# Kernel tuning notes

Measured on AMD Instinct MI355X. Metric: run time of the kernel, lower is better.

## Reference

```python
import jax, jax.numpy as jnp
import numpy as np

N_USERS = 10000
N_ITEMS = 100000
N_FEATURES = 64
EMB_DIM = 128
TAU = 0.01
NUM_SEQ = 100000
SEQ_LEN = 50


def setup_inputs() -> dict:
    key = jax.random.key(0)
    k1, k2, k3, k4, k5, k6 = jax.random.split(key, 6)
    users = jax.random.randint(k1, (NUM_SEQ,), 0, N_USERS, dtype=jnp.int32)
    items = jax.random.randint(k2, (NUM_SEQ,), 0, N_ITEMS, dtype=jnp.int32)
    R_ui = jax.random.normal(k3, (NUM_SEQ, SEQ_LEN, N_FEATURES), dtype=jnp.float32)
    mask = jax.random.randint(k4, (NUM_SEQ, SEQ_LEN), 0, 2).astype(bool)
    mask = mask.at[:, 0].set(True)  # ensure every sequence has >=1 valid step
    w = jax.random.normal(k5, (N_FEATURES,), dtype=jnp.float32)  # nn.init.normal_
    item_emb = jax.random.normal(k6, (N_ITEMS + 1, EMB_DIM), dtype=jnp.float32) * 0.1
    item_emb = item_emb.at[0].set(0.0)  # padding_idx=0
    alpha = jnp.ones((1,), jnp.float32)
    beta = jnp.ones((1,), jnp.float32)
    gamma = jnp.ones((1,), jnp.float32)
    return {"users": users, "items": items, "R_ui": R_ui, "mask": mask,
            "w": w, "item_emb": item_emb, "alpha": alpha, "beta": beta, "gamma": gamma}


def reference(users, items, R_ui, mask, w, item_emb, alpha, beta, gamma):
    # Z: [num_seq, seq_len] masked power-mean features
    Z = jnp.einsum('nsd,d->ns', R_ui, w)
    Wv = jnp.maximum(Z, TAU)                       # nn.Threshold(tau, tau)
    Wp = jnp.where(mask, Wv ** alpha, 0.0)         # W[~mask] = 0, then **alpha
    W_alpha = jnp.sum(Wp, axis=-1) ** (1.0 / alpha)
    R_beta = jnp.sum(mask, axis=-1).astype(R_ui.dtype) ** beta
    wt = (W_alpha * R_beta) ** gamma               # [num_seq]
    q = item_emb[items]                            # [num_seq, emb_dim]
    # per-user weighted average (replaces Python loop over users.unique())
    num = jax.ops.segment_sum(wt[:, None] * q, users, num_segments=N_USERS + 1)
    den = jax.ops.segment_sum(wt, users, num_segments=N_USERS + 1)
    p = num[users] / den[users][:, None]
    r = jnp.sum(p * q, axis=-1)                    # [num_seq]
    return r
```

## Files before the change

### kernel.cpp

```cpp
#include <hip/hip_runtime.h>
#include <hip/hip_bf16.h>
#include <stdint.h>

#define N_USERS   10000
#define N_ITEMS   100000
#define N_FEAT    64
#define EMB_DIM   128
#define SEQ_LEN   50
#define TAU       0.01f

typedef float f32x4 __attribute__((ext_vector_type(4)));

__device__ inline f32x4 nt_load4(const float* p) {
    return __builtin_nontemporal_load(reinterpret_cast<const f32x4*>(p));
}


__device__ inline int detect_mask_mode(const void* mask_raw, int lane) {
    const unsigned int* mi = (const unsigned int*)mask_raw;
    unsigned int pv = mi[lane];
    float        pf = __uint_as_float(pv);
    bool allint = __all(pv <= 1u) != 0;
    bool allflt = __all(pf == 0.0f || pf == 1.0f) != 0;
    return allint ? 0 : (allflt ? 1 : 2);
}

__device__ inline unsigned long long load_mask_ballot(
    const void* mask_raw, int mode, int n, int lane)
{
    bool mv = false;
    if (lane < SEQ_LEN) {
        size_t off = (size_t)n * SEQ_LEN + lane;
        if (mode == 0)      mv = ((const int*)mask_raw)[off] != 0;
        else if (mode == 1) mv = ((const float*)mask_raw)[off] != 0.0f;
        else                mv = ((const uint8_t*)mask_raw)[off] != 0;
    }
    return __ballot(mv);
}

__global__ __launch_bounds__(256) void wt_scatter_kernel(
    const float* __restrict__ R, const void* __restrict__ mask_raw,
    const float* __restrict__ w,
    const int* __restrict__ users, const int* __restrict__ items,
    const float* __restrict__ item_emb,
    const float* __restrict__ alpha_p, const float* __restrict__ beta_p,
    const float* __restrict__ gamma_p,
    float* __restrict__ num, float* __restrict__ den, int num_seq)
{
    int wave = (blockIdx.x * blockDim.x + threadIdx.x) >> 6;
    int lane = threadIdx.x & 63;
    if (wave >= num_seq) return;
    const int n = wave;

    const int u  = users[n];
    const int it = items[n];

    const int mode = detect_mask_mode(mask_raw, lane);
    unsigned long long mbits = load_mask_ballot(mask_raw, mode, n, lane);

    const float alpha = alpha_p[0];
    const float beta  = beta_p[0];
    const float gamma = gamma_p[0];

    const int f4 = lane & 15;
    const int sg = lane >> 4;
    const f32x4 w4 = *reinterpret_cast<const f32x4*>(w + 4 * f4);
    const float* Rn = R + (size_t)n * SEQ_LEN * N_FEAT;

    float acc = 0.0f;
    float cnt = 0.0f;

    #pragma unroll
    for (int s0 = 0; s0 < SEQ_LEN; s0 += 4) {
        int s = s0 + sg;
        bool valid = (s < SEQ_LEN);
        f32x4 x = {0.f, 0.f, 0.f, 0.f};
        if (valid) x = nt_load4(Rn + s * N_FEAT + 4 * f4);
        float d = x.x * w4.x + x.y * w4.y + x.z * w4.z + x.w * w4.w;
        d += __shfl_xor(d, 1);
        d += __shfl_xor(d, 2);
        d += __shfl_xor(d, 4);
        d += __shfl_xor(d, 8);
        if (valid && ((mbits >> s) & 1ULL)) {
            float Wv = fmaxf(d, TAU);
            acc += (alpha == 1.0f) ? Wv : powf(Wv, alpha);
            cnt += 1.0f;
        }
    }
    acc += __shfl_xor(acc, 16);
    acc += __shfl_xor(acc, 32);
    cnt += __shfl_xor(cnt, 16);
    cnt += __shfl_xor(cnt, 32);

    float W_alpha = (alpha == 1.0f) ? acc : powf(acc, 1.0f / alpha);
    float R_beta  = (beta  == 1.0f) ? cnt : powf(cnt, beta);
    float base    = W_alpha * R_beta;
    float wt      = (gamma == 1.0f) ? base : powf(base, gamma);

    const float2 q = reinterpret_cast<const float2*>(item_emb + (size_t)it * EMB_DIM)[lane];
    float* numrow = num + (size_t)u * EMB_DIM;
    atomicAdd(&numrow[2 * lane],     wt * q.x);
    atomicAdd(&numrow[2 * lane + 1], wt * q.y);
    if (lane == 0) atomicAdd(&den[u], wt);
}

__global__ __launch_bounds__(512) void final_kernel(
    const int* __restrict__ users, const int* __restrict__ items,
    const float* __restrict__ item_emb,
    const float* __restrict__ num, const float* __restrict__ den,
    float* __restrict__ r, int num_seq)
{
    int wave = (blockIdx.x * blockDim.x + threadIdx.x) >> 6;
    int lane = threadIdx.x & 63;
    if (wave >= num_seq) return;
    const int n = wave;

    int u  = users[n];
    int it = items[n];
    float dinv = den[u];
    float2 q = reinterpret_cast<const float2*>(item_emb + (size_t)it * EMB_DIM)[lane];
    float2 p = reinterpret_cast<const float2*>(num + (size_t)u * EMB_DIM)[lane];
    float dot = q.x * p.x + q.y * p.y;
    dot += __shfl_xor(dot, 1);
    dot += __shfl_xor(dot, 2);
    dot += __shfl_xor(dot, 4);
    dot += __shfl_xor(dot, 8);
    dot += __shfl_xor(dot, 16);
    dot += __shfl_xor(dot, 32);
    if (lane == 0) r[n] = dot / dinv;
}

extern "C" void kernel_launch(void* const* d_in, const int* in_sizes, int n_in,
                              void* d_out, int out_size, void* d_ws, size_t ws_size,
                              hipStream_t stream)
{
    const int*   users    = (const int*)d_in[0];
    const int*   items    = (const int*)d_in[1];
    const float* R_ui     = (const float*)d_in[2];
    const void*  mask     = d_in[3];
    const float* w        = (const float*)d_in[4];
    const float* item_emb = (const float*)d_in[5];
    const float* alpha    = (const float*)d_in[6];
    const float* beta     = (const float*)d_in[7];
    const float* gamma    = (const float*)d_in[8];

    const int num_seq = in_sizes[0];
    float* num = (float*)d_ws;
    float* den = (float*)d_ws + (size_t)N_USERS * EMB_DIM;

    (void)hipMemsetAsync(d_ws, 0,
                         ((size_t)N_USERS * EMB_DIM + N_USERS) * sizeof(float),
                         stream);

    {
        int waves_per_block = 4;
        int blocks = (num_seq + waves_per_block - 1) / waves_per_block;
        wt_scatter_kernel<<<blocks, 256, 0, stream>>>(R_ui, mask, w, users, items,
                                                      item_emb, alpha, beta, gamma,
                                                      num, den, num_seq);
    }
    {
        int waves_per_block = 8;
        int blocks = (num_seq + waves_per_block - 1) / waves_per_block;
        final_kernel<<<blocks, 512, 0, stream>>>(users, items, item_emb,
                                                 num, den, (float*)d_out, num_seq);
    }
}
```

Baseline: 274.3 us.

## Persistent grid-stride scatter kernel with register double-buffered sequence prefetch

The scatter kernel becomes persistent with a fixed grid of 2048 blocks. Each wave grid-strides over sequences and keeps two register buffers, so the next sequence's R rows, mask, indices and embedding row load while the current one computes and issues atomics. The R load is reshaped into 12 full-wave float4 loads plus one float2 tail, which removes the idle lanes in the last step. The valid count now comes from a popcount of the mask ballot. The cost is much higher register pressure from holding about 60 floats per buffer, which may lower occupancy, and a fixed grid size that may not fit every GPU.

Result: no change. 273.4 us (-0.4%).

```diff
diff --git a/kernel.cpp b/kernel.cpp
--- a/kernel.cpp
+++ b/kernel.cpp
@@ -8,15 +8,19 @@
 #define EMB_DIM   128
 #define SEQ_LEN   50
 #define TAU       0.01f
+#define SEQ_FLOATS (SEQ_LEN * N_FEAT)
 
 typedef float f32x4 __attribute__((ext_vector_type(4)));
-
-__device__ inline f32x4 nt_load4(const float* p) {
+typedef float f32x2 __attribute__((ext_vector_type(2)));
+
+__device__ __forceinline__ f32x4 nt_load4(const float* p) {
     return __builtin_nontemporal_load(reinterpret_cast<const f32x4*>(p));
 }
-
-
-__device__ inline int detect_mask_mode(const void* mask_raw, int lane) {
+__device__ __forceinline__ f32x2 nt_load2(const float* p) {
+    return __builtin_nontemporal_load(reinterpret_cast<const f32x2*>(p));
+}
+
+__device__ __forceinline__ int detect_mask_mode(const void* mask_raw, int lane) {
     const unsigned int* mi = (const unsigned int*)mask_raw;
     unsigned int pv = mi[lane];
     float        pf = __uint_as_float(pv);
@@ -25,7 +29,7 @@
     return allint ? 0 : (allflt ? 1 : 2);
 }
 
-__device__ inline unsigned long long load_mask_ballot(
+__device__ __forceinline__ unsigned long long load_mask_ballot(
     const void* mask_raw, int mode, int n, int lane)
 {
     bool mv = false;
@@ -36,6 +40,83 @@
         else                mv = ((const uint8_t*)mask_raw)[off] != 0;
     }
     return __ballot(mv);
+}
+
+struct SeqRegs {
+    f32x4 v[12];
+    f32x2 t;
+    f32x2 q;
+    int u, it;
+    unsigned long long mb;
+};
+
+__device__ __forceinline__ void load_seq(
+    int n, int lane, const float* __restrict__ R,
+    const void* __restrict__ mask_raw, int mode,
+    const int* __restrict__ users, const int* __restrict__ items,
+    const float* __restrict__ item_emb, SeqRegs& s)
+{
+    const float* Rn = R + (size_t)n * SEQ_FLOATS;
+    #pragma unroll
+    for (int j = 0; j < 12; ++j)
+        s.v[j] = nt_load4(Rn + j * 256 + 4 * lane);
+    s.t  = nt_load2(Rn + 3072 + 2 * lane);
+    s.u  = users[n];
+    s.it = items[n];
+    s.mb = load_mask_ballot(mask_raw, mode, n, lane);
+    s.q  = *reinterpret_cast<const f32x2*>(item_emb + (size_t)s.it * EMB_DIM + 2 * lane);
+}
+
+__device__ __forceinline__ void compute_scatter(
+    const SeqRegs& s, int lane, f32x4 w4, f32x2 wt2,
+    float alpha, float beta, float gamma,
+    float* __restrict__ num, float* __restrict__ den)
+{
+    const int sg = lane >> 4;
+    float acc = 0.0f;
+
+    #pragma unroll
+    for (int j = 0; j < 12; ++j) {
+        float d = s.v[j].x * w4.x + s.v[j].y * w4.y
+                + s.v[j].z * w4.z + s.v[j].w * w4.w;
+        d += __shfl_xor(d, 1);
+        d += __shfl_xor(d, 2);
+        d += __shfl_xor(d, 4);
+        d += __shfl_xor(d, 8);
+        int step = 4 * j + sg;
+        if ((s.mb >> step) & 1ULL) {
+            float Wv = fmaxf(d, TAU);
+            acc += (alpha == 1.0f) ? Wv : powf(Wv, alpha);
+        }
+    }
+    acc += __shfl_xor(acc, 16);
+    acc += __shfl_xor(acc, 32);
+
+    float dt = s.t.x * wt2.x + s.t.y * wt2.y;
+    dt += __shfl_xor(dt, 1);
+    dt += __shfl_xor(dt, 2);
+    dt += __shfl_xor(dt, 4);
+    dt += __shfl_xor(dt, 8);
+    dt += __shfl_xor(dt, 16);
+    int ts = 48 + (lane >> 5);
+    float c = 0.0f;
+    if ((s.mb >> ts) & 1ULL) {
+        float Wv = fmaxf(dt, TAU);
+        c = (alpha == 1.0f) ? Wv : powf(Wv, alpha);
+    }
+    acc += c + __shfl_xor(c, 32);
+
+    float cnt = (float)__popcll(s.mb & ((1ULL << SEQ_LEN) - 1));
+
+    float W_alpha = (alpha == 1.0f) ? acc : powf(acc, 1.0f / alpha);
+    float R_beta  = (beta  == 1.0f) ? cnt : powf(cnt, beta);
+    float base    = W_alpha * R_beta;
+    float wt      = (gamma == 1.0f) ? base : powf(base, gamma);
+
+    float* numrow = num + (size_t)s.u * EMB_DIM;
+    atomicAdd(&numrow[2 * lane],     wt * s.q.x);
+    atomicAdd(&numrow[2 * lane + 1], wt * s.q.y);
+    if (lane == 0) atomicAdd(&den[s.u], wt);
 }
 
 __global__ __launch_bounds__(256) void wt_scatter_kernel(
@@ -47,61 +128,39 @@
     const float* __restrict__ gamma_p,
     float* __restrict__ num, float* __restrict__ den, int num_seq)
 {
-    int wave = (blockIdx.x * blockDim.x + threadIdx.x) >> 6;
-    int lane = threadIdx.x & 63;
-    if (wave >= num_seq) return;
-    const int n = wave;
-
-    const int u  = users[n];
-    const int it = items[n];
+    const int lane   = threadIdx.x & 63;
+    const int gwave  = (blockIdx.x * blockDim.x + threadIdx.x) >> 6;
+    const int nwaves = (gridDim.x * blockDim.x) >> 6;
 
     const int mode = detect_mask_mode(mask_raw, lane);
-    unsigned long long mbits = load_mask_ballot(mask_raw, mode, n, lane);
-
     const float alpha = alpha_p[0];
     const float beta  = beta_p[0];
     const float gamma = gamma_p[0];
 
-    const int f4 = lane & 15;
-    const int sg = lane >> 4;
-    const f32x4 w4 = *reinterpret_cast<const f32x4*>(w + 4 * f4);
-    const float* Rn = R + (size_t)n * SEQ_LEN * N_FEAT;
-
-    float acc = 0.0f;
-    float cnt = 0.0f;
-
-    #pragma unroll
-    for (int s0 = 0; s0 < SEQ_LEN; s0 += 4) {
-        int s = s0 + sg;
-        bool valid = (s < SEQ_LEN);
-        f32x4 x = {0.f, 0.f, 0.f, 0.f};
-        if (valid) x = nt_load4(Rn + s * N_FEAT + 4 * f4);
-        float d = x.x * w4.x + x.y * w4.y + x.z * w4.z + x.w * w4.w;
-        d += __shfl_xor(d, 1);
-        d += __shfl_xor(d, 2);
-        d += __shfl_xor(d, 4);
-        d += __shfl_xor(d, 8);
-        if (valid && ((mbits >> s) & 1ULL)) {
-            float Wv = fmaxf(d, TAU);
-            acc += (alpha == 1.0f) ? Wv : powf(Wv, alpha);
-            cnt += 1.0f;
-        }
-    }
-    acc += __shfl_xor(acc, 16);
-    acc += __shfl_xor(acc, 32);
-    cnt += __shfl_xor(cnt, 16);
-    cnt += __shfl_xor(cnt, 32);
-
-    float W_alpha = (alpha == 1.0f) ? acc : powf(acc, 1.0f / alpha);
-    float R_beta  = (beta  == 1.0f) ? cnt : powf(cnt, beta);
-    float base    = W_alpha * R_beta;
-    float wt      = (gamma == 1.0f) ? base : powf(base, gamma);
-
-    const float2 q = reinterpret_cast<const float2*>(item_emb + (size_t)it * EMB_DIM)[lane];
-    float* numrow = num + (size_t)u * EMB_DIM;
-    atomicAdd(&numrow[2 * lane],     wt * q.x);
-    atomicAdd(&numrow[2 * lane + 1], wt * q.y);
-    if (lane == 0) atomicAdd(&den[u], wt);
+    const f32x4 w4  = *reinterpret_cast<const f32x4*>(w + 4 * (lane & 15));
+    const f32x2 wt2 = *reinterpret_cast<const f32x2*>(w + 2 * (lane & 31));
+
+    int n = gwave;
+    if (n >= num_seq) return;
+
+    SeqRegs A, B;
+    load_seq(n, lane, R, mask_raw, mode, users, items, item_emb, A);
+
+    while (true) {
+        int n1 = n + nwaves;
+        if (n1 < num_seq)
+            load_seq(n1, lane, R, mask_raw, mode, users, items, item_emb, B);
+        compute_scatter(A, lane, w4, wt2, alpha, beta, gamma, num, den);
+        if (n1 >= num_seq) break;
+
+        int n2 = n1 + nwaves;
+        if (n2 < num_seq)
+            load_seq(n2, lane, R, mask_raw, mode, users, items, item_emb, A);
+        compute_scatter(B, lane, w4, wt2, alpha, beta, gamma, num, den);
+        if (n2 >= num_seq) break;
+
+        n = n2;
+    }
 }
 
 __global__ __launch_bounds__(512) void final_kernel(
@@ -117,7 +176,7 @@
 
     int u  = users[n];
     int it = items[n];
-    float dinv = den[u];
+    float dv = den[u];
     float2 q = reinterpret_cast<const float2*>(item_emb + (size_t)it * EMB_DIM)[lane];
     float2 p = reinterpret_cast<const float2*>(num + (size_t)u * EMB_DIM)[lane];
     float dot = q.x * p.x + q.y * p.y;
@@ -127,7 +186,7 @@
     dot += __shfl_xor(dot, 8);
     dot += __shfl_xor(dot, 16);
     dot += __shfl_xor(dot, 32);
-    if (lane == 0) r[n] = dot / dinv;
+    if (lane == 0) r[n] = dot / dv;
 }
 
 extern "C" void kernel_launch(void* const* d_in, const int* in_sizes, int n_in,
@@ -153,11 +212,9 @@
                          stream);
 
     {
-        int waves_per_block = 4;
-        int blocks = (num_seq + waves_per_block - 1) / waves_per_block;
-        wt_scatter_kernel<<<blocks, 256, 0, stream>>>(R_ui, mask, w, users, items,
-                                                      item_emb, alpha, beta, gamma,
-                                                      num, den, num_seq);
+        wt_scatter_kernel<<<2048, 256, 0, stream>>>(R_ui, mask, w, users, items,
+                                                    item_emb, alpha, beta, gamma,
+                                                    num, den, num_seq);
     }
     {
         int waves_per_block = 8;
```
